# Kernel optimization log

Hardware: AMD Instinct MI355X
Metric: run time of the kernel (lower is better)

The kernel has to match this reference:

```python
import jax, jax.numpy as jnp
import numpy as np

B, S, NB = 8, 512, 23
INIT, E, R, T = 512, 256, 3, 2
NEG = -9e8

def _gru(x, h, wih, whh, bih, bhh):
    gi = x @ wih.T + bih
    gh = h @ whh.T + bhh
    ir, iz, inn = jnp.split(gi, 3, axis=-1)
    hr, hz, hn = jnp.split(gh, 3, axis=-1)
    r = jax.nn.sigmoid(ir + hr)
    z = jax.nn.sigmoid(iz + hz)
    n = jnp.tanh(inn + r * hn)
    return (1.0 - z) * n + z * h

def setup_inputs():
    key = jax.random.key(0)
    ks = jax.random.split(key, 30)
    def lin(k, o, i):
        return jax.random.normal(k, (o, i), jnp.float32) * 0.02
    def vec(k, n):
        return jax.random.normal(k, (n,), jnp.float32) * 0.02
    inp = {}
    inp["amino_list"] = jax.random.normal(ks[0], (B, S, INIT), jnp.float32)
    inp["amino_mask"] = (jax.random.uniform(ks[1], (B, S)) < 0.9).astype(jnp.float32)
    inp["emb_W"] = lin(ks[2], E, INIT); inp["emb_b"] = vec(ks[3], E)
    inp["nb_W"] = lin(ks[4], E, INIT); inp["nb_b"] = vec(ks[5], E)
    inp["align_W"] = jax.random.normal(ks[6], (R, 1, 2 * E), jnp.float32) * 0.02
    inp["align_b"] = jax.random.normal(ks[7], (R, 1), jnp.float32) * 0.02
    inp["attend_W"] = jax.random.normal(ks[8], (R, E, E), jnp.float32) * 0.02
    inp["attend_b"] = jax.random.normal(ks[9], (R, E), jnp.float32) * 0.02
    inp["gru_wih"] = jax.random.normal(ks[10], (R, 3 * E, E), jnp.float32) * 0.02
    inp["gru_whh"] = jax.random.normal(ks[11], (R, 3 * E, E), jnp.float32) * 0.02
    inp["gru_bih"] = jax.random.normal(ks[12], (R, 3 * E), jnp.float32) * 0.02
    inp["gru_bhh"] = jax.random.normal(ks[13], (R, 3 * E), jnp.float32) * 0.02
    inp["seq_align_W"] = lin(ks[14], 1, 2 * E); inp["seq_align_b"] = vec(ks[15], 1)
    inp["seq_attend_W"] = lin(ks[16], E, E); inp["seq_attend_b"] = vec(ks[17], E)
    inp["seq_gru_wih"] = lin(ks[18], 3 * E, E); inp["seq_gru_bih"] = vec(ks[19], 3 * E)
    inp["seq_gru_whh"] = lin(ks[20], 3 * E, E); inp["seq_gru_bhh"] = vec(ks[21], 3 * E)
    inp["amino_degree_list"] = jax.random.randint(ks[22], (B, S, NB), -1, S)
    return inp

def reference(amino_list, amino_mask, emb_W, emb_b, nb_W, nb_b, align_W, align_b,
              attend_W, attend_b, gru_wih, gru_whh, gru_bih, gru_bhh,
              seq_align_W, seq_align_b, seq_attend_W, seq_attend_b,
              seq_gru_wih, seq_gru_whh, seq_gru_bih, seq_gru_bhh, amino_degree_list):
    idx = amino_degree_list
    lrelu = jax.nn.leaky_relu
    # per-batch neighbor gather: (S,D),(S,NB) -> (S,NB,D); index -1 wraps (masked out below)
    gather = jax.vmap(lambda f, i: f[i])
    feat = lrelu(amino_list @ emb_W.T + emb_b)               # (B,S,E)
    nfeat = lrelu(gather(amino_list, idx) @ nb_W.T + nb_b)   # (B,S,NB,E)
    attend_mask = (idx != -1).astype(feat.dtype)             # (B,S,NB)
    smask = jnp.where(idx == -1, NEG, 0.0).astype(feat.dtype)

    def attn(d, center, nbr):
        # align Linear on concat([center, nbr]) split into two matvecs (same math, no concat)
        aW = align_W[d, 0]
        score = lrelu(jnp.einsum('bse,e->bs', center, aW[:E])[:, :, None]
                      + jnp.einsum('bsne,e->bsn', nbr, aW[E:]) + align_b[d, 0])
        w = jax.nn.softmax(score + smask, axis=-1) * attend_mask   # softmax over neighbor axis
        nt = nbr @ attend_W[d].T + attend_b[d]
        return jax.nn.elu(jnp.einsum('bsn,bsne->bse', w, nt))

    h = _gru(attn(0, feat, nfeat).reshape(-1, E), feat.reshape(-1, E),
             gru_wih[0], gru_whh[0], gru_bih[0], gru_bhh[0])
    act = jax.nn.relu(h.reshape(B, S, E))
    for d in range(1, R):
        ctx = attn(d, act, gather(act, idx))
        h = _gru(ctx.reshape(-1, E), h, gru_wih[d], gru_whh[d], gru_bih[d], gru_bhh[d])
        act = jax.nn.relu(h.reshape(B, S, E))

    seq_feature = jnp.sum(act * amino_mask[:, :, None], axis=1)  # (B,E)
    act_mol = jax.nn.relu(seq_feature)                           # fixed across T (as in torch)
    seq_smask = jnp.where(amino_mask == 0, NEG, 0.0)
    saW = seq_align_W[0]
    act_seq = act_mol
    for _ in range(T):
        score = lrelu((act_mol @ saW[:E])[:, None]
                      + jnp.einsum('bse,e->bs', act, saW[E:]) + seq_align_b[0])
        w = jax.nn.softmax(score + seq_smask, axis=-1) * amino_mask  # softmax over seq axis
        tf = act @ seq_attend_W.T + seq_attend_b
        seq_ctx = jax.nn.elu(jnp.einsum('bs,bse->be', w, tf))
        seq_feature = _gru(seq_ctx, seq_feature, seq_gru_wih, seq_gru_whh, seq_gru_bih, seq_gru_bhh)
        act_seq = jax.nn.relu(seq_feature)
    return (act_seq, act)
```

## Files before the change

### kernel.cpp

```cpp
#include <hip/hip_runtime.h>
#include <math.h>


#define BSZ   8
#define SEQ   512
#define NBR   23
#define EMB   256
#define INITD 512
#define BS    (BSZ*SEQ)
#define G3    (3*EMB)
#define NEGV  -9e8f

typedef __attribute__((ext_vector_type(8))) short short8;
typedef __attribute__((ext_vector_type(4))) float f32x4;

__device__ __forceinline__ float lrelu(float x){ return x > 0.f ? x : 0.01f*x; }
__device__ __forceinline__ float elu1 (float x){ return x > 0.f ? x : (expf(x)-1.f); }
__device__ __forceinline__ float sigm (float x){ return 1.f/(1.f+expf(-x)); }
__device__ __forceinline__ float bf2f(ushort u){
    union { unsigned int i; float f; } v; v.i = ((unsigned int)u) << 16; return v.f;
}
__device__ __forceinline__ ushort f2bf(float f){
    union { float f; unsigned int i; } v; v.f = f;
    unsigned int u = v.i;
    return (ushort)((u + 0x7FFFu + ((u >> 16) & 1u)) >> 16);
}

struct GemmLds { ushort A[2][64][64]; ushort W[2][64][64]; };

__global__ __launch_bounds__(256) void convert7_kernel(
    const float* s0, ushort* d0, int n0,
    const float* s1, ushort* d1, int n1,
    const float* s2, ushort* d2, int n2,
    const float* s3, ushort* d3, int n3,
    const float* s4, ushort* d4, int n4,
    const float* s5, ushort* d5, int n5,
    const float* s6, ushort* d6, int n6)
{
    const float* srcs[7] = {s0,s1,s2,s3,s4,s5,s6};
    ushort* dsts[7] = {d0,d1,d2,d3,d4,d5,d6};
    int ns[7] = {n0,n1,n2,n3,n4,n5,n6};
    int seg = blockIdx.y;
    const float* s = srcs[seg]; ushort* d = dsts[seg]; int n = ns[seg];
    size_t i = ((size_t)blockIdx.x * 256 + threadIdx.x) * 8;
    size_t stride = (size_t)gridDim.x * 256 * 8;
    for (; i < (size_t)n; i += stride) {
        float4 a = *reinterpret_cast<const float4*>(s + i);
        float4 b = *reinterpret_cast<const float4*>(s + i + 4);
        uint4 o;
        o.x = (unsigned)f2bf(a.x) | ((unsigned)f2bf(a.y) << 16);
        o.y = (unsigned)f2bf(a.z) | ((unsigned)f2bf(a.w) << 16);
        o.z = (unsigned)f2bf(b.x) | ((unsigned)f2bf(b.y) << 16);
        o.w = (unsigned)f2bf(b.z) | ((unsigned)f2bf(b.w) << 16);
        *reinterpret_cast<uint4*>(d + i) = o;
    }
}

template<int ACT, bool WF32, bool WBF>
__device__ __forceinline__ void gemm_dev(
    const ushort* __restrict__ A, const ushort* __restrict__ W,
    const float* __restrict__ bias,
    float* __restrict__ C, ushort* __restrict__ Cbf,
    int N, int K, int bx, int by, GemmLds& L)
{
    const int tid = threadIdx.x;
    const int m0 = bx * 64, n0 = by * 64;
    const int wv = tid >> 6, lane = tid & 63;
    const int fr = lane & 15, grp = lane >> 4;
    const int lrow = tid >> 3, lc8 = tid & 7;
    const int kc = K >> 3;
    const int sw = lc8 ^ (lrow & 7);

    f32x4 acc[4];
    #pragma unroll
    for (int c = 0; c < 4; ++c) acc[c] = (f32x4){0.f, 0.f, 0.f, 0.f};

    const float4* A4 = reinterpret_cast<const float4*>(A);
    const float4* W4 = reinterpret_cast<const float4*>(W);

    float4 a0 = A4[(size_t)(m0 + lrow)      * kc + lc8];
    float4 a1 = A4[(size_t)(m0 + lrow + 32) * kc + lc8];
    float4 w0 = W4[(size_t)(n0 + lrow)      * kc + lc8];
    float4 w1 = W4[(size_t)(n0 + lrow + 32) * kc + lc8];
    *reinterpret_cast<float4*>(&L.A[0][lrow     ][sw << 3]) = a0;
    *reinterpret_cast<float4*>(&L.A[0][lrow + 32][sw << 3]) = a1;
    *reinterpret_cast<float4*>(&L.W[0][lrow     ][sw << 3]) = w0;
    *reinterpret_cast<float4*>(&L.W[0][lrow + 32][sw << 3]) = w1;
    __syncthreads();

    const int ar = (wv << 4) + fr;
    int cur = 0;
    for (int k0 = 64; k0 < K; k0 += 64) {
        a0 = A4[(size_t)(m0 + lrow)      * kc + (k0 >> 3) + lc8];
        a1 = A4[(size_t)(m0 + lrow + 32) * kc + (k0 >> 3) + lc8];
        w0 = W4[(size_t)(n0 + lrow)      * kc + (k0 >> 3) + lc8];
        w1 = W4[(size_t)(n0 + lrow + 32) * kc + (k0 >> 3) + lc8];
        #pragma unroll
        for (int ks = 0; ks < 2; ++ks) {
            short8 af = *reinterpret_cast<const short8*>(
                &L.A[cur][ar][((((ks << 2) + grp) ^ (ar & 7)) << 3)]);
            #pragma unroll
            for (int c = 0; c < 4; ++c) {
                const int br = (c << 4) + fr;
                short8 bv = *reinterpret_cast<const short8*>(
                    &L.W[cur][br][((((ks << 2) + grp) ^ (br & 7)) << 3)]);
                acc[c] = __builtin_amdgcn_mfma_f32_16x16x32_bf16(af, bv, acc[c], 0, 0, 0);
            }
        }
        *reinterpret_cast<float4*>(&L.A[cur^1][lrow     ][sw << 3]) = a0;
        *reinterpret_cast<float4*>(&L.A[cur^1][lrow + 32][sw << 3]) = a1;
        *reinterpret_cast<float4*>(&L.W[cur^1][lrow     ][sw << 3]) = w0;
        *reinterpret_cast<float4*>(&L.W[cur^1][lrow + 32][sw << 3]) = w1;
        __syncthreads();
        cur ^= 1;
    }
    #pragma unroll
    for (int ks = 0; ks < 2; ++ks) {
        short8 af = *reinterpret_cast<const short8*>(
            &L.A[cur][ar][((((ks << 2) + grp) ^ (ar & 7)) << 3)]);
        #pragma unroll
        for (int c = 0; c < 4; ++c) {
            const int br = (c << 4) + fr;
            short8 bv = *reinterpret_cast<const short8*>(
                &L.W[cur][br][((((ks << 2) + grp) ^ (br & 7)) << 3)]);
            acc[c] = __builtin_amdgcn_mfma_f32_16x16x32_bf16(af, bv, acc[c], 0, 0, 0);
        }
    }

    const int mrow = m0 + (wv << 4) + (grp << 2);
    #pragma unroll
    for (int c = 0; c < 4; ++c) {
        const int n = n0 + (c << 4) + fr;
        const float bv = bias[n];
        #pragma unroll
        for (int j = 0; j < 4; ++j) {
            float t = acc[c][j] + bv;
            if (ACT == 1) t = lrelu(t);
            size_t off = (size_t)(mrow + j) * N + n;
            if (WF32) C[off] = t;
            if (WBF)  Cbf[off] = f2bf(t);
        }
    }
}

template<int ACT, bool WF32, bool WBF>
__global__ __launch_bounds__(256) void gemm_mfma(
    const ushort* __restrict__ A, const ushort* __restrict__ W,
    const float* __restrict__ bias,
    float* __restrict__ C, ushort* __restrict__ Cbf, int N, int K)
{
    __shared__ GemmLds L;
    gemm_dev<ACT,WF32,WBF>(A, W, bias, C, Cbf, N, K, blockIdx.x, blockIdx.y, L);
}

__global__ __launch_bounds__(256) void featnbase_kernel(
    const ushort* __restrict__ aminobf,
    const ushort* __restrict__ embWbf, const float* __restrict__ embB,
    float* __restrict__ feat, ushort* __restrict__ featbf,
    const ushort* __restrict__ nbWbf, const float* __restrict__ nbB,
    float* __restrict__ nbase, ushort* __restrict__ nbasebf)
{
    __shared__ GemmLds L;
    int blk = blockIdx.x;
    if (blk < 256)
        gemm_dev<1,true,true>(aminobf, embWbf, embB, feat, featbf, EMB, INITD, blk & 63, blk >> 6, L);
    else {
        blk -= 256;
        gemm_dev<1,true,true>(aminobf, nbWbf, nbB, nbase, nbasebf, EMB, INITD, blk & 63, blk >> 6, L);
    }
}

__global__ __launch_bounds__(256) void round_pre_kernel(
    const ushort* __restrict__ nbrbf, const ushort* __restrict__ attWd,
    const float* __restrict__ attBd, ushort* __restrict__ ntb,
    const ushort* __restrict__ hprevbf, const ushort* __restrict__ gwhhd,
    const float* __restrict__ gbhhd, float* __restrict__ gh,
    const float* __restrict__ center, const float* __restrict__ nbrbase,
    const float* __restrict__ alignWd,
    float* __restrict__ cdot, float* __restrict__ ndot)
{
    __shared__ GemmLds L;
    int blk = blockIdx.x;
    if (blk < 256) {
        gemm_dev<0,false,true>(nbrbf, attWd, attBd, nullptr, ntb, EMB, EMB, blk & 63, blk >> 6, L);
    } else if (blk < 1024) {
        int b = blk - 256;
        gemm_dev<0,true,false>(hprevbf, gwhhd, gbhhd, gh, nullptr, G3, EMB, b & 63, b >> 6, L);
    } else {
        const int b    = blk - 1024;
        const int lane = threadIdx.x & 63;
        const int wv   = threadIdx.x >> 6;
        const int e    = lane << 2;
        const int rb   = b * 16 + wv * 4;
        float4 w0 = *reinterpret_cast<const float4*>(&alignWd[e]);
        float4 w1 = *reinterpret_cast<const float4*>(&alignWd[EMB + e]);
        #pragma unroll
        for (int i = 0; i < 4; ++i) {
            const int r = rb + i;
            float4 xc = *reinterpret_cast<const float4*>(&center[(size_t)r*EMB + e]);
            float4 xn = *reinterpret_cast<const float4*>(&nbrbase[(size_t)r*EMB + e]);
            float ac = xc.x*w0.x + xc.y*w0.y + xc.z*w0.z + xc.w*w0.w;
            float an = xn.x*w1.x + xn.y*w1.y + xn.z*w1.z + xn.w*w1.w;
            #pragma unroll
            for (int off = 32; off; off >>= 1) {
                ac += __shfl_xor(ac, off, 64);
                an += __shfl_xor(an, off, 64);
            }
            if (lane == 0) { cdot[r] = ac; ndot[r] = an; }
        }
    }
}

__global__ __launch_bounds__(256) void attn_kernel(
    const float* __restrict__ cdot, const float* __restrict__ ndot,
    const int* __restrict__ idx, const ushort* __restrict__ nt,
    const float* __restrict__ alignB, ushort* __restrict__ ctxbf)
{
    const int r   = blockIdx.x;
    const int b   = r >> 9;
    const int tid = threadIdx.x;
    __shared__ float w_s[NBR];
    __shared__ float vm_s[NBR];
    __shared__ int   row_s[NBR];
    __shared__ float red[2];
    if (tid < NBR) {
        int j = idx[(size_t)r*NBR + tid];
        int valid = (j >= 0);
        int jj = valid ? j : j + SEQ;
        int row = b*SEQ + jj;
        row_s[tid] = row;
        vm_s[tid]  = (float)valid;
        float sc = lrelu(cdot[r] + ndot[row] + alignB[0]);
        w_s[tid] = sc + (valid ? 0.f : NEGV);
    }
    __syncthreads();
    if (tid == 0) {
        float m = w_s[0];
        for (int n = 1; n < NBR; ++n) m = fmaxf(m, w_s[n]);
        red[0] = m;
    }
    __syncthreads();
    if (tid < NBR) w_s[tid] = expf(w_s[tid] - red[0]);
    __syncthreads();
    if (tid == 0) {
        float s = 0.f;
        for (int n = 0; n < NBR; ++n) s += w_s[n];
        red[1] = 1.f / s;
    }
    __syncthreads();
    if (tid < NBR) w_s[tid] *= red[1] * vm_s[tid];
    __syncthreads();
    float acc = 0.f;
    #pragma unroll 1
    for (int n = 0; n < NBR; ++n)
        acc += w_s[n] * bf2f(nt[(size_t)row_s[n]*EMB + tid]);
    ctxbf[(size_t)r*EMB + tid] = f2bf(elu1(acc));
}

__global__ __launch_bounds__(256) void gru_kernel(
    const float* __restrict__ gi, const float* __restrict__ gh,
    const float* __restrict__ hprev,
    float* __restrict__ hout, ushort* __restrict__ hbf,
    float* __restrict__ actout, ushort* __restrict__ actbf)
{
    const size_t r = blockIdx.x * 4 + (threadIdx.x >> 6);
    const int    e = (threadIdx.x & 63) << 2;
    const size_t gb = r*G3 + e, hb = r*EMB + e;
    float4 ir4 = *reinterpret_cast<const float4*>(&gi[gb]);
    float4 iz4 = *reinterpret_cast<const float4*>(&gi[gb + EMB]);
    float4 in4 = *reinterpret_cast<const float4*>(&gi[gb + 2*EMB]);
    float4 hr4 = *reinterpret_cast<const float4*>(&gh[gb]);
    float4 hz4 = *reinterpret_cast<const float4*>(&gh[gb + EMB]);
    float4 hn4 = *reinterpret_cast<const float4*>(&gh[gb + 2*EMB]);
    float4 hp4 = *reinterpret_cast<const float4*>(&hprev[hb]);
    float hv[4], av[4];
    const float ir_[4] = {ir4.x,ir4.y,ir4.z,ir4.w}, iz_[4] = {iz4.x,iz4.y,iz4.z,iz4.w},
                in_[4] = {in4.x,in4.y,in4.z,in4.w}, hr_[4] = {hr4.x,hr4.y,hr4.z,hr4.w},
                hz_[4] = {hz4.x,hz4.y,hz4.z,hz4.w}, hn_[4] = {hn4.x,hn4.y,hn4.z,hn4.w},
                hp_[4] = {hp4.x,hp4.y,hp4.z,hp4.w};
    #pragma unroll
    for (int i = 0; i < 4; ++i) {
        float rg = sigm(ir_[i] + hr_[i]);
        float z  = sigm(iz_[i] + hz_[i]);
        float n  = tanhf(in_[i] + rg*hn_[i]);
        hv[i] = (1.f - z)*n + z*hp_[i];
        av[i] = fmaxf(hv[i], 0.f);
    }
    *reinterpret_cast<float4*>(&hout[hb])   = make_float4(hv[0],hv[1],hv[2],hv[3]);
    *reinterpret_cast<float4*>(&actout[hb]) = make_float4(av[0],av[1],av[2],av[3]);
    uint2 hp, ap;
    hp.x = (unsigned)f2bf(hv[0]) | ((unsigned)f2bf(hv[1]) << 16);
    hp.y = (unsigned)f2bf(hv[2]) | ((unsigned)f2bf(hv[3]) << 16);
    ap.x = (unsigned)f2bf(av[0]) | ((unsigned)f2bf(av[1]) << 16);
    ap.y = (unsigned)f2bf(av[2]) | ((unsigned)f2bf(av[3]) << 16);
    *reinterpret_cast<uint2*>(&hbf[hb])  = hp;
    *reinterpret_cast<uint2*>(&actbf[hb]) = ap;
}

__global__ __launch_bounds__(256) void seqpre_kernel(
    const ushort* __restrict__ actbf, const ushort* __restrict__ satWbf,
    const float* __restrict__ satB, float* __restrict__ tf,
    const float* __restrict__ act, const float* __restrict__ mask,
    const float* __restrict__ saW,
    float* __restrict__ seqfeat, float* __restrict__ cmol,
    float* __restrict__ ad)
{
    __shared__ GemmLds L;
    int blk = blockIdx.x;
    if (blk < 256) {
        gemm_dev<0,true,false>(actbf, satWbf, satB, tf, nullptr, EMB, EMB, blk & 63, blk >> 6, L);
    } else if (blk < 264) {
        const int b = blk - 256;
        const int e = threadIdx.x;
        float acc = 0.f;
        for (int s = 0; s < SEQ; ++s)
            acc += act[((size_t)b*SEQ + s)*EMB + e] * mask[b*SEQ + s];
        seqfeat[b*EMB + e] = acc;
        float* red = reinterpret_cast<float*>(&L);
        red[e] = fmaxf(acc, 0.f) * saW[e];
        __syncthreads();
        for (int off = 128; off; off >>= 1) {
            if (e < off) red[e] += red[e + off];
            __syncthreads();
        }
        if (e == 0) cmol[b] = red[0];
    } else {
        const int b2   = blk - 264;
        const int lane = threadIdx.x & 63;
        const int wv   = threadIdx.x >> 6;
        const int e    = lane << 2;
        const int rb   = b2 * 16 + wv * 4;
        float4 w1 = *reinterpret_cast<const float4*>(&saW[EMB + e]);
        #pragma unroll
        for (int i = 0; i < 4; ++i) {
            const int r = rb + i;
            float4 xa = *reinterpret_cast<const float4*>(&act[(size_t)r*EMB + e]);
            float an = xa.x*w1.x + xa.y*w1.y + xa.z*w1.z + xa.w*w1.w;
            #pragma unroll
            for (int off = 32; off; off >>= 1) an += __shfl_xor(an, off, 64);
            if (lane == 0) ad[r] = an;
        }
    }
}

__global__ __launch_bounds__(512) void seqsoftmax_kernel(
    const float* __restrict__ ad, const float* __restrict__ mask,
    const float* __restrict__ saB, const float* __restrict__ cmol,
    float* __restrict__ wvec)
{
    const int b = blockIdx.x;
    const int s = threadIdx.x;
    __shared__ float red[SEQ];
    float mk = mask[b*SEQ + s];
    float sc = lrelu(cmol[b] + ad[b*SEQ + s] + saB[0]) + (mk == 0.f ? NEGV : 0.f);
    red[s] = sc; __syncthreads();
    for (int off = 256; off; off >>= 1) {
        if (s < off) red[s] = fmaxf(red[s], red[s + off]);
        __syncthreads();
    }
    float m = red[0]; __syncthreads();
    float ev = expf(sc - m);
    red[s] = ev; __syncthreads();
    for (int off = 256; off; off >>= 1) {
        if (s < off) red[s] += red[s + off];
        __syncthreads();
    }
    wvec[b*SEQ + s] = ev / red[0] * mk;
}

__global__ __launch_bounds__(256) void seqpv_kernel(
    const float* __restrict__ wvec, const float* __restrict__ tf,
    float* __restrict__ partial)
{
    const int st = blockIdx.x, b = blockIdx.y;
    const int e  = threadIdx.x;
    float acc = 0.f;
    const int s0 = st * 32;
    #pragma unroll 4
    for (int s = s0; s < s0 + 32; ++s)
        acc += wvec[b*SEQ + s] * tf[((size_t)b*SEQ + s)*EMB + e];
    partial[((size_t)b*16 + st)*EMB + e] = acc;
}

__global__ __launch_bounds__(256) void seqfinish_kernel(
    const float* __restrict__ partial, float* __restrict__ seqctx)
{
    const int b = blockIdx.x, e = threadIdx.x;
    float acc = 0.f;
    #pragma unroll
    for (int st = 0; st < 16; ++st)
        acc += partial[((size_t)b*16 + st)*EMB + e];
    seqctx[(size_t)b*EMB + e] = elu1(acc);
}

__global__ __launch_bounds__(256) void matvec8_kernel(
    const float* __restrict__ X, const float* __restrict__ Wm,
    const float* __restrict__ bias, float* __restrict__ Y)
{
    const int g    = blockIdx.x * 4 + (threadIdx.x >> 6);
    const int b    = blockIdx.y;
    const int lane = threadIdx.x & 63;
    float4 w = *reinterpret_cast<const float4*>(&Wm[(size_t)g*EMB + (lane << 2)]);
    float4 x = *reinterpret_cast<const float4*>(&X[(size_t)b*EMB + (lane << 2)]);
    float d = w.x*x.x + w.y*x.y + w.z*x.z + w.w*x.w;
    #pragma unroll
    for (int off = 32; off; off >>= 1) d += __shfl_xor(d, off, 64);
    if (lane == 0) Y[(size_t)b*G3 + g] = d + bias[g];
}

__global__ __launch_bounds__(256) void seqgru_el_kernel(
    const float* __restrict__ sgi, const float* __restrict__ sgh,
    const float* __restrict__ sfin,
    float* __restrict__ sfout, float* __restrict__ actseq)
{
    const int b = blockIdx.x;
    const int e = threadIdx.x;
    float rg = sigm(sgi[b*G3 + e]       + sgh[b*G3 + e]);
    float z  = sigm(sgi[b*G3 + EMB + e] + sgh[b*G3 + EMB + e]);
    float n  = tanhf(sgi[b*G3 + 2*EMB + e] + rg * sgh[b*G3 + 2*EMB + e]);
    float hp = sfin[b*EMB + e];
    float hv = (1.f - z)*n + z*hp;
    sfout[b*EMB + e]  = hv;
    actseq[b*EMB + e] = fmaxf(hv, 0.f);
}

extern "C" void kernel_launch(void* const* d_in, const int* in_sizes, int n_in,
                              void* d_out, int out_size, void* d_ws, size_t ws_size,
                              hipStream_t stream) {
    (void)in_sizes; (void)n_in; (void)out_size; (void)ws_size;
    const float* amino  = (const float*)d_in[0];
    const float* mask   = (const float*)d_in[1];
    const float* embW   = (const float*)d_in[2];
    const float* embB   = (const float*)d_in[3];
    const float* nbW    = (const float*)d_in[4];
    const float* nbB    = (const float*)d_in[5];
    const float* alignW = (const float*)d_in[6];
    const float* alignB = (const float*)d_in[7];
    const float* attW   = (const float*)d_in[8];
    const float* attB   = (const float*)d_in[9];
    const float* gwih   = (const float*)d_in[10];
    const float* gwhh   = (const float*)d_in[11];
    const float* gbih   = (const float*)d_in[12];
    const float* gbhh   = (const float*)d_in[13];
    const float* saW    = (const float*)d_in[14];
    const float* saB    = (const float*)d_in[15];
    const float* satW   = (const float*)d_in[16];
    const float* satB   = (const float*)d_in[17];
    const float* sgwih  = (const float*)d_in[18];
    const float* sgbih  = (const float*)d_in[19];
    const float* sgwhh  = (const float*)d_in[20];
    const float* sgbhh  = (const float*)d_in[21];
    const int*   idx    = (const int*)d_in[22];

    char* cur = (char*)d_ws;
    auto alloc = [&](size_t bytes) -> char* {
        char* p = cur; cur += (bytes + 255) & ~(size_t)255; return p;
    };
    float* feat    = (float*)alloc((size_t)BS*EMB*4);
    float* nbase   = (float*)alloc((size_t)BS*EMB*4);
    float* h       = (float*)alloc((size_t)BS*EMB*4);
    float* gi      = (float*)alloc((size_t)BS*G3*4);
    float* gh      = (float*)alloc((size_t)BS*G3*4);
    float* cdot    = (float*)alloc(BS*4);
    float* ndot    = (float*)alloc(BS*4);
    float* seqfeat = (float*)alloc(BSZ*EMB*4);
    float* cmol    = (float*)alloc(64*4);
    float* seqctx  = (float*)alloc(BSZ*EMB*4);
    float* sgi     = (float*)alloc(BSZ*G3*4);
    float* sgh     = (float*)alloc(BSZ*G3*4);
    float* partial = (float*)alloc((size_t)BSZ*16*EMB*4);
    ushort* featbf  = (ushort*)alloc((size_t)BS*EMB*2);
    ushort* nbasebf = (ushort*)alloc((size_t)BS*EMB*2);
    ushort* actbf   = (ushort*)alloc((size_t)BS*EMB*2);
    ushort* hbf     = (ushort*)alloc((size_t)BS*EMB*2);
    ushort* ctxbf   = (ushort*)alloc((size_t)BS*EMB*2);
    ushort* ntb     = (ushort*)alloc((size_t)BS*EMB*2);
    ushort* embWbf  = (ushort*)alloc((size_t)EMB*INITD*2);
    ushort* nbWbf   = (ushort*)alloc((size_t)EMB*INITD*2);
    ushort* attWbf  = (ushort*)alloc((size_t)3*EMB*EMB*2);
    ushort* gwihbf  = (ushort*)alloc((size_t)3*G3*EMB*2);
    ushort* gwhhbf  = (ushort*)alloc((size_t)3*G3*EMB*2);
    ushort* satWbf  = (ushort*)alloc((size_t)EMB*EMB*2);
    ushort* aminobf = (ushort*)gi;
    float*  tf      = gi;
    float*  ad      = cdot;
    float*  wvec    = ndot;

    float* out    = (float*)d_out;
    float* actseq = out;
    float* act    = out + BSZ*EMB;

    convert7_kernel<<<dim3(1024, 7), 256, 0, stream>>>(
        amino, aminobf, BS*INITD,
        embW,  embWbf,  EMB*INITD,
        nbW,   nbWbf,   EMB*INITD,
        attW,  attWbf,  3*EMB*EMB,
        gwih,  gwihbf,  3*G3*EMB,
        gwhh,  gwhhbf,  3*G3*EMB,
        satW,  satWbf,  EMB*EMB);

    featnbase_kernel<<<512, 256, 0, stream>>>(
        aminobf, embWbf, embB, feat, featbf, nbWbf, nbB, nbase, nbasebf);

    for (int d = 0; d < 3; ++d) {
        const float*  center   = (d == 0) ? feat    : act;
        const float*  nbrbase  = (d == 0) ? nbase   : act;
        const ushort* nbrbf    = (d == 0) ? nbasebf : actbf;
        const float*  hprev    = (d == 0) ? feat    : h;
        const ushort* hprevbf  = (d == 0) ? featbf  : hbf;
        round_pre_kernel<<<1280, 256, 0, stream>>>(
            nbrbf, attWbf + (size_t)d*EMB*EMB, attB + d*EMB, ntb,
            hprevbf, gwhhbf + (size_t)d*G3*EMB, gbhh + d*G3, gh,
            center, nbrbase, alignW + d*2*EMB, cdot, ndot);
        attn_kernel<<<BS, 256, 0, stream>>>(cdot, ndot, idx, ntb, alignB + d, ctxbf);
        gemm_mfma<0,true,false><<<dim3(64, 12), 256, 0, stream>>>(
            ctxbf, gwihbf + (size_t)d*G3*EMB, gbih + d*G3, gi, nullptr, G3, EMB);
        gru_kernel<<<BS/4, 256, 0, stream>>>(gi, gh, hprev, h, hbf, act, actbf);
    }

    seqpre_kernel<<<520, 256, 0, stream>>>(
        actbf, satWbf, satB, tf, act, mask, saW, seqfeat, cmol, ad);
    seqsoftmax_kernel<<<BSZ, 512, 0, stream>>>(ad, mask, saB, cmol, wvec);
    seqpv_kernel<<<dim3(16, BSZ), 256, 0, stream>>>(wvec, tf, partial);
    seqfinish_kernel<<<BSZ, 256, 0, stream>>>(partial, seqctx);
    matvec8_kernel<<<dim3(G3/4, BSZ), 256, 0, stream>>>(seqctx, sgwih, sgbih, sgi);
    for (int t = 0; t < 2; ++t) {
        matvec8_kernel<<<dim3(G3/4, BSZ), 256, 0, stream>>>(seqfeat, sgwhh, sgbhh, sgh);
        seqgru_el_kernel<<<BSZ, 256, 0, stream>>>(sgi, sgh, seqfeat, seqfeat, actseq);
    }
}
```

Measured before the change: 184.2 us.

## Store GRU gates in bf16, warp-per-row attention, fuse sequence tail kernels

The gi/gh gate buffers are now written and read in bf16 instead of fp32, halving the traffic of the largest intermediates. The neighbour-attention kernel now processes four rows per block, one wavefront per row, using shuffles instead of shared-memory serial reductions, and reads vectorised ushort4 values. The sequence-level tail merges softmax, PV and finish into fewer kernels, and replaces the matvec/GRU chain with two fused seqstep kernels that use bf16 weights converted up front. Together these cut launch count and memory traffic, at the cost of extra bf16 rounding on the gate pre-activations and the sequence GRU weights.

```diff
diff --git a/kernel.cpp b/kernel.cpp
--- a/kernel.cpp
+++ b/kernel.cpp
@@ -28,18 +28,20 @@
 
 struct GemmLds { ushort A[2][64][64]; ushort W[2][64][64]; };
 
-__global__ __launch_bounds__(256) void convert7_kernel(
+__global__ __launch_bounds__(256) void convert9_kernel(
     const float* s0, ushort* d0, int n0,
     const float* s1, ushort* d1, int n1,
     const float* s2, ushort* d2, int n2,
     const float* s3, ushort* d3, int n3,
     const float* s4, ushort* d4, int n4,
     const float* s5, ushort* d5, int n5,
-    const float* s6, ushort* d6, int n6)
-{
-    const float* srcs[7] = {s0,s1,s2,s3,s4,s5,s6};
-    ushort* dsts[7] = {d0,d1,d2,d3,d4,d5,d6};
-    int ns[7] = {n0,n1,n2,n3,n4,n5,n6};
+    const float* s6, ushort* d6, int n6,
+    const float* s7, ushort* d7, int n7,
+    const float* s8, ushort* d8, int n8)
+{
+    const float* srcs[9] = {s0,s1,s2,s3,s4,s5,s6,s7,s8};
+    ushort* dsts[9] = {d0,d1,d2,d3,d4,d5,d6,d7,d8};
+    int ns[9] = {n0,n1,n2,n3,n4,n5,n6,n7,n8};
     int seg = blockIdx.y;
     const float* s = srcs[seg]; ushort* d = dsts[seg]; int n = ns[seg];
     size_t i = ((size_t)blockIdx.x * 256 + threadIdx.x) * 8;
@@ -174,7 +176,7 @@
     const ushort* __restrict__ nbrbf, const ushort* __restrict__ attWd,
     const float* __restrict__ attBd, ushort* __restrict__ ntb,
     const ushort* __restrict__ hprevbf, const ushort* __restrict__ gwhhd,
-    const float* __restrict__ gbhhd, float* __restrict__ gh,
+    const float* __restrict__ gbhhd, ushort* __restrict__ ghbf,
     const float* __restrict__ center, const float* __restrict__ nbrbase,
     const float* __restrict__ alignWd,
     float* __restrict__ cdot, float* __restrict__ ndot)
@@ -185,7 +187,7 @@
         gemm_dev<0,false,true>(nbrbf, attWd, attBd, nullptr, ntb, EMB, EMB, blk & 63, blk >> 6, L);
     } else if (blk < 1024) {
         int b = blk - 256;
-        gemm_dev<0,true,false>(hprevbf, gwhhd, gbhhd, gh, nullptr, G3, EMB, b & 63, b >> 6, L);
+        gemm_dev<0,false,true>(hprevbf, gwhhd, gbhhd, nullptr, ghbf, G3, EMB, b & 63, b >> 6, L);
     } else {
         const int b    = blk - 1024;
         const int lane = threadIdx.x & 63;
@@ -216,49 +218,44 @@
     const int* __restrict__ idx, const ushort* __restrict__ nt,
     const float* __restrict__ alignB, ushort* __restrict__ ctxbf)
 {
-    const int r   = blockIdx.x;
-    const int b   = r >> 9;
-    const int tid = threadIdx.x;
-    __shared__ float w_s[NBR];
-    __shared__ float vm_s[NBR];
-    __shared__ int   row_s[NBR];
-    __shared__ float red[2];
-    if (tid < NBR) {
-        int j = idx[(size_t)r*NBR + tid];
+    const int lane = threadIdx.x & 63;
+    const int r = blockIdx.x * 4 + (threadIdx.x >> 6);
+    const int b = r >> 9;
+    float sc = -3e38f, vm = 0.f; int row = 0;
+    if (lane < NBR) {
+        int j = idx[(size_t)r*NBR + lane];
         int valid = (j >= 0);
         int jj = valid ? j : j + SEQ;
-        int row = b*SEQ + jj;
-        row_s[tid] = row;
-        vm_s[tid]  = (float)valid;
-        float sc = lrelu(cdot[r] + ndot[row] + alignB[0]);
-        w_s[tid] = sc + (valid ? 0.f : NEGV);
-    }
-    __syncthreads();
-    if (tid == 0) {
-        float m = w_s[0];
-        for (int n = 1; n < NBR; ++n) m = fmaxf(m, w_s[n]);
-        red[0] = m;
-    }
-    __syncthreads();
-    if (tid < NBR) w_s[tid] = expf(w_s[tid] - red[0]);
-    __syncthreads();
-    if (tid == 0) {
-        float s = 0.f;
-        for (int n = 0; n < NBR; ++n) s += w_s[n];
-        red[1] = 1.f / s;
-    }
-    __syncthreads();
-    if (tid < NBR) w_s[tid] *= red[1] * vm_s[tid];
-    __syncthreads();
-    float acc = 0.f;
+        row = b*SEQ + jj;
+        vm = (float)valid;
+        sc = lrelu(cdot[r] + ndot[row] + alignB[0]) + (valid ? 0.f : NEGV);
+    }
+    float m = sc;
+    #pragma unroll
+    for (int off = 32; off; off >>= 1) m = fmaxf(m, __shfl_xor(m, off, 64));
+    float ev = (lane < NBR) ? expf(sc - m) : 0.f;
+    float s = ev;
+    #pragma unroll
+    for (int off = 32; off; off >>= 1) s += __shfl_xor(s, off, 64);
+    float wgt = ev * vm / s;
+    float acc0 = 0.f, acc1 = 0.f, acc2 = 0.f, acc3 = 0.f;
+    const int e = lane << 2;
     #pragma unroll 1
-    for (int n = 0; n < NBR; ++n)
-        acc += w_s[n] * bf2f(nt[(size_t)row_s[n]*EMB + tid]);
-    ctxbf[(size_t)r*EMB + tid] = f2bf(elu1(acc));
+    for (int n = 0; n < NBR; ++n) {
+        float wn = __shfl(wgt, n, 64);
+        int   rn = __shfl(row, n, 64);
+        ushort4 v = *reinterpret_cast<const ushort4*>(&nt[(size_t)rn*EMB + e]);
+        acc0 += wn * bf2f(v.x); acc1 += wn * bf2f(v.y);
+        acc2 += wn * bf2f(v.z); acc3 += wn * bf2f(v.w);
+    }
+    uint2 o;
+    o.x = (unsigned)f2bf(elu1(acc0)) | ((unsigned)f2bf(elu1(acc1)) << 16);
+    o.y = (unsigned)f2bf(elu1(acc2)) | ((unsigned)f2bf(elu1(acc3)) << 16);
+    *reinterpret_cast<uint2*>(&ctxbf[(size_t)r*EMB + e]) = o;
 }
 
 __global__ __launch_bounds__(256) void gru_kernel(
-    const float* __restrict__ gi, const float* __restrict__ gh,
+    const ushort* __restrict__ gibf, const ushort* __restrict__ ghbf,
     const float* __restrict__ hprev,
     float* __restrict__ hout, ushort* __restrict__ hbf,
     float* __restrict__ actout, ushort* __restrict__ actbf)
@@ -266,18 +263,21 @@
     const size_t r = blockIdx.x * 4 + (threadIdx.x >> 6);
     const int    e = (threadIdx.x & 63) << 2;
     const size_t gb = r*G3 + e, hb = r*EMB + e;
-    float4 ir4 = *reinterpret_cast<const float4*>(&gi[gb]);
-    float4 iz4 = *reinterpret_cast<const float4*>(&gi[gb + EMB]);
-    float4 in4 = *reinterpret_cast<const float4*>(&gi[gb + 2*EMB]);
-    float4 hr4 = *reinterpret_cast<const float4*>(&gh[gb]);
-    float4 hz4 = *reinterpret_cast<const float4*>(&gh[gb + EMB]);
-    float4 hn4 = *reinterpret_cast<const float4*>(&gh[gb + 2*EMB]);
+    ushort4 ir4 = *reinterpret_cast<const ushort4*>(&gibf[gb]);
+    ushort4 iz4 = *reinterpret_cast<const ushort4*>(&gibf[gb + EMB]);
+    ushort4 in4 = *reinterpret_cast<const ushort4*>(&gibf[gb + 2*EMB]);
+    ushort4 hr4 = *reinterpret_cast<const ushort4*>(&ghbf[gb]);
+    ushort4 hz4 = *reinterpret_cast<const ushort4*>(&ghbf[gb + EMB]);
+    ushort4 hn4 = *reinterpret_cast<const ushort4*>(&ghbf[gb + 2*EMB]);
     float4 hp4 = *reinterpret_cast<const float4*>(&hprev[hb]);
+    const float ir_[4] = {bf2f(ir4.x),bf2f(ir4.y),bf2f(ir4.z),bf2f(ir4.w)};
+    const float iz_[4] = {bf2f(iz4.x),bf2f(iz4.y),bf2f(iz4.z),bf2f(iz4.w)};
+    const float in_[4] = {bf2f(in4.x),bf2f(in4.y),bf2f(in4.z),bf2f(in4.w)};
+    const float hr_[4] = {bf2f(hr4.x),bf2f(hr4.y),bf2f(hr4.z),bf2f(hr4.w)};
+    const float hz_[4] = {bf2f(hz4.x),bf2f(hz4.y),bf2f(hz4.z),bf2f(hz4.w)};
+    const float hn_[4] = {bf2f(hn4.x),bf2f(hn4.y),bf2f(hn4.z),bf2f(hn4.w)};
+    const float hp_[4] = {hp4.x,hp4.y,hp4.z,hp4.w};
     float hv[4], av[4];
-    const float ir_[4] = {ir4.x,ir4.y,ir4.z,ir4.w}, iz_[4] = {iz4.x,iz4.y,iz4.z,iz4.w},
-                in_[4] = {in4.x,in4.y,in4.z,in4.w}, hr_[4] = {hr4.x,hr4.y,hr4.z,hr4.w},
-                hz_[4] = {hz4.x,hz4.y,hz4.z,hz4.w}, hn_[4] = {hn4.x,hn4.y,hn4.z,hn4.w},
-                hp_[4] = {hp4.x,hp4.y,hp4.z,hp4.w};
     #pragma unroll
     for (int i = 0; i < 4; ++i) {
         float rg = sigm(ir_[i] + hr_[i]);
@@ -293,7 +293,7 @@
     hp.y = (unsigned)f2bf(hv[2]) | ((unsigned)f2bf(hv[3]) << 16);
     ap.x = (unsigned)f2bf(av[0]) | ((unsigned)f2bf(av[1]) << 16);
     ap.y = (unsigned)f2bf(av[2]) | ((unsigned)f2bf(av[3]) << 16);
-    *reinterpret_cast<uint2*>(&hbf[hb])  = hp;
+    *reinterpret_cast<uint2*>(&hbf[hb])   = hp;
     *reinterpret_cast<uint2*>(&actbf[hb]) = ap;
 }
 
@@ -343,85 +343,106 @@
     }
 }
 
-__global__ __launch_bounds__(512) void seqsoftmax_kernel(
+__global__ __launch_bounds__(256) void seqpv2_kernel(
     const float* __restrict__ ad, const float* __restrict__ mask,
     const float* __restrict__ saB, const float* __restrict__ cmol,
-    float* __restrict__ wvec)
-{
-    const int b = blockIdx.x;
-    const int s = threadIdx.x;
-    __shared__ float red[SEQ];
-    float mk = mask[b*SEQ + s];
-    float sc = lrelu(cmol[b] + ad[b*SEQ + s] + saB[0]) + (mk == 0.f ? NEGV : 0.f);
-    red[s] = sc; __syncthreads();
-    for (int off = 256; off; off >>= 1) {
-        if (s < off) red[s] = fmaxf(red[s], red[s + off]);
+    const float* __restrict__ tf, float* __restrict__ partial)
+{
+    const int st = blockIdx.x, b = blockIdx.y;
+    const int tid = threadIdx.x;
+    __shared__ float w_s[SEQ];
+    __shared__ float red[256];
+    float mk0 = mask[b*SEQ + tid], mk1 = mask[b*SEQ + 256 + tid];
+    float cb = cmol[b], bb = saB[0];
+    float s0 = lrelu(cb + ad[b*SEQ + tid] + bb)       + (mk0 == 0.f ? NEGV : 0.f);
+    float s1 = lrelu(cb + ad[b*SEQ + 256 + tid] + bb) + (mk1 == 0.f ? NEGV : 0.f);
+    red[tid] = fmaxf(s0, s1); __syncthreads();
+    for (int off = 128; off; off >>= 1) {
+        if (tid < off) red[tid] = fmaxf(red[tid], red[tid + off]);
         __syncthreads();
     }
     float m = red[0]; __syncthreads();
-    float ev = expf(sc - m);
-    red[s] = ev; __syncthreads();
-    for (int off = 256; off; off >>= 1) {
-        if (s < off) red[s] += red[s + off];
+    float e0 = expf(s0 - m), e1 = expf(s1 - m);
+    red[tid] = e0 + e1; __syncthreads();
+    for (int off = 128; off; off >>= 1) {
+        if (tid < off) red[tid] += red[tid + off];
         __syncthreads();
     }
-    wvec[b*SEQ + s] = ev / red[0] * mk;
-}
-
-__global__ __launch_bounds__(256) void seqpv_kernel(
-    const float* __restrict__ wvec, const float* __restrict__ tf,
-    float* __restrict__ partial)
-{
-    const int st = blockIdx.x, b = blockIdx.y;
-    const int e  = threadIdx.x;
+    float inv = 1.f / red[0];
+    w_s[tid]       = e0 * inv * mk0;
+    w_s[tid + 256] = e1 * inv * mk1;
+    __syncthreads();
     float acc = 0.f;
-    const int s0 = st * 32;
+    const int s0i = st * 32;
     #pragma unroll 4
-    for (int s = s0; s < s0 + 32; ++s)
-        acc += wvec[b*SEQ + s] * tf[((size_t)b*SEQ + s)*EMB + e];
-    partial[((size_t)b*16 + st)*EMB + e] = acc;
-}
-
-__global__ __launch_bounds__(256) void seqfinish_kernel(
-    const float* __restrict__ partial, float* __restrict__ seqctx)
-{
-    const int b = blockIdx.x, e = threadIdx.x;
-    float acc = 0.f;
-    #pragma unroll
-    for (int st = 0; st < 16; ++st)
-        acc += partial[((size_t)b*16 + st)*EMB + e];
-    seqctx[(size_t)b*EMB + e] = elu1(acc);
-}
-
-__global__ __launch_bounds__(256) void matvec8_kernel(
-    const float* __restrict__ X, const float* __restrict__ Wm,
-    const float* __restrict__ bias, float* __restrict__ Y)
-{
-    const int g    = blockIdx.x * 4 + (threadIdx.x >> 6);
-    const int b    = blockIdx.y;
-    const int lane = threadIdx.x & 63;
-    float4 w = *reinterpret_cast<const float4*>(&Wm[(size_t)g*EMB + (lane << 2)]);
-    float4 x = *reinterpret_cast<const float4*>(&X[(size_t)b*EMB + (lane << 2)]);
-    float d = w.x*x.x + w.y*x.y + w.z*x.z + w.w*x.w;
-    #pragma unroll
-    for (int off = 32; off; off >>= 1) d += __shfl_xor(d, off, 64);
-    if (lane == 0) Y[(size_t)b*G3 + g] = d + bias[g];
-}
-
-__global__ __launch_bounds__(256) void seqgru_el_kernel(
-    const float* __restrict__ sgi, const float* __restrict__ sgh,
-    const float* __restrict__ sfin,
-    float* __restrict__ sfout, float* __restrict__ actseq)
-{
-    const int b = blockIdx.x;
-    const int e = threadIdx.x;
-    float rg = sigm(sgi[b*G3 + e]       + sgh[b*G3 + e]);
-    float z  = sigm(sgi[b*G3 + EMB + e] + sgh[b*G3 + EMB + e]);
-    float n  = tanhf(sgi[b*G3 + 2*EMB + e] + rg * sgh[b*G3 + 2*EMB + e]);
-    float hp = sfin[b*EMB + e];
-    float hv = (1.f - z)*n + z*hp;
-    sfout[b*EMB + e]  = hv;
-    actseq[b*EMB + e] = fmaxf(hv, 0.f);
+    for (int s = s0i; s < s0i + 32; ++s)
+        acc += w_s[s] * tf[((size_t)b*SEQ + s)*EMB + tid];
+    partial[((size_t)b*16 + st)*EMB + tid] = acc;
+}
+
+template<int T0>
+__global__ __launch_bounds__(512) void seqstep_kernel(
+    const float* __restrict__ partial, const float* __restrict__ sfin,
+    const ushort* __restrict__ sgwihbf, const float* __restrict__ sgbih,
+    const ushort* __restrict__ sgwhhbf, const float* __restrict__ sgbhh,
+    float* __restrict__ sgi, float* __restrict__ sfout,
+    float* __restrict__ actseq)
+{
+    const int b = blockIdx.x >> 2, q = blockIdx.x & 3;
+    const int tid = threadIdx.x, lane = tid & 63, wv = tid >> 6;
+    __shared__ float xs[EMB];
+    __shared__ float hs[EMB];
+    __shared__ float gis[192], ghs[192];
+    if (tid < EMB) {
+        hs[tid] = sfin[b*EMB + tid];
+        if (T0) {
+            float a = 0.f;
+            #pragma unroll
+            for (int st = 0; st < 16; ++st)
+                a += partial[((size_t)b*16 + st)*EMB + tid];
+            xs[tid] = elu1(a);
+        }
+    }
+    if (!T0) {
+        for (int l = tid; l < 192; l += 512) {
+            int g = (l >> 6)*EMB + (q << 6) + (l & 63);
+            gis[l] = sgi[b*G3 + g];
+        }
+    }
+    __syncthreads();
+    const int nrows = T0 ? 384 : 192;
+    const int rpw = nrows >> 3;
+    for (int i = 0; i < rpw; ++i) {
+        const int l = wv * rpw + i;
+        const int iswih = T0 && (l < 192);
+        const int ll = (T0 && l >= 192) ? l - 192 : l;
+        const int g = (ll >> 6)*EMB + (q << 6) + (ll & 63);
+        const ushort* Wm = iswih ? sgwihbf : sgwhhbf;
+        ushort4 w4 = *reinterpret_cast<const ushort4*>(&Wm[(size_t)g*EMB + (lane << 2)]);
+        float4 x4 = *reinterpret_cast<const float4*>(iswih ? &xs[lane << 2] : &hs[lane << 2]);
+        float d = bf2f(w4.x)*x4.x + bf2f(w4.y)*x4.y + bf2f(w4.z)*x4.z + bf2f(w4.w)*x4.w;
+        #pragma unroll
+        for (int off = 32; off; off >>= 1) d += __shfl_xor(d, off, 64);
+        if (lane == 0) {
+            if (iswih) {
+                d += sgbih[g];
+                gis[ll] = d;
+                sgi[b*G3 + g] = d;
+            } else {
+                ghs[ll] = d + sgbhh[g];
+            }
+        }
+    }
+    __syncthreads();
+    if (tid < 64) {
+        const int e = (q << 6) + tid;
+        float rg = sigm(gis[tid]       + ghs[tid]);
+        float z  = sigm(gis[64 + tid]  + ghs[64 + tid]);
+        float n  = tanhf(gis[128 + tid] + rg*ghs[128 + tid]);
+        float hv = (1.f - z)*n + z*hs[e];
+        sfout[b*EMB + e]  = hv;
+        actseq[b*EMB + e] = fmaxf(hv, 0.f);
+    }
 }
 
 extern "C" void kernel_launch(void* const* d_in, const int* in_sizes, int n_in,
@@ -459,45 +480,47 @@
     float* feat    = (float*)alloc((size_t)BS*EMB*4);
     float* nbase   = (float*)alloc((size_t)BS*EMB*4);
     float* h       = (float*)alloc((size_t)BS*EMB*4);
-    float* gi      = (float*)alloc((size_t)BS*G3*4);
-    float* gh      = (float*)alloc((size_t)BS*G3*4);
+    float* tf      = (float*)alloc((size_t)BS*EMB*4);
     float* cdot    = (float*)alloc(BS*4);
     float* ndot    = (float*)alloc(BS*4);
+    float* ad      = (float*)alloc(BS*4);
     float* seqfeat = (float*)alloc(BSZ*EMB*4);
+    float* sf2     = (float*)alloc(BSZ*EMB*4);
     float* cmol    = (float*)alloc(64*4);
-    float* seqctx  = (float*)alloc(BSZ*EMB*4);
     float* sgi     = (float*)alloc(BSZ*G3*4);
-    float* sgh     = (float*)alloc(BSZ*G3*4);
     float* partial = (float*)alloc((size_t)BSZ*16*EMB*4);
+    ushort* aminobf = (ushort*)alloc((size_t)BS*INITD*2);
     ushort* featbf  = (ushort*)alloc((size_t)BS*EMB*2);
     ushort* nbasebf = (ushort*)alloc((size_t)BS*EMB*2);
     ushort* actbf   = (ushort*)alloc((size_t)BS*EMB*2);
     ushort* hbf     = (ushort*)alloc((size_t)BS*EMB*2);
     ushort* ctxbf   = (ushort*)alloc((size_t)BS*EMB*2);
     ushort* ntb     = (ushort*)alloc((size_t)BS*EMB*2);
+    ushort* gibf    = (ushort*)alloc((size_t)BS*G3*2);
+    ushort* ghbf    = (ushort*)alloc((size_t)BS*G3*2);
     ushort* embWbf  = (ushort*)alloc((size_t)EMB*INITD*2);
     ushort* nbWbf   = (ushort*)alloc((size_t)EMB*INITD*2);
     ushort* attWbf  = (ushort*)alloc((size_t)3*EMB*EMB*2);
     ushort* gwihbf  = (ushort*)alloc((size_t)3*G3*EMB*2);
     ushort* gwhhbf  = (ushort*)alloc((size_t)3*G3*EMB*2);
     ushort* satWbf  = (ushort*)alloc((size_t)EMB*EMB*2);
-    ushort* aminobf = (ushort*)gi;
-    float*  tf      = gi;
-    float*  ad      = cdot;
-    float*  wvec    = ndot;
+    ushort* sgwihbf = (ushort*)alloc((size_t)G3*EMB*2);
+    ushort* sgwhhbf = (ushort*)alloc((size_t)G3*EMB*2);
 
     float* out    = (float*)d_out;
     float* actseq = out;
     float* act    = out + BSZ*EMB;
 
-    convert7_kernel<<<dim3(1024, 7), 256, 0, stream>>>(
+    convert9_kernel<<<dim3(1024, 9), 256, 0, stream>>>(
         amino, aminobf, BS*INITD,
         embW,  embWbf,  EMB*INITD,
         nbW,   nbWbf,   EMB*INITD,
         attW,  attWbf,  3*EMB*EMB,
         gwih,  gwihbf,  3*G3*EMB,
         gwhh,  gwhhbf,  3*G3*EMB,
-        satW,  satWbf,  EMB*EMB);
+        satW,  satWbf,  EMB*EMB,
+        sgwih, sgwihbf, G3*EMB,
+        sgwhh, sgwhhbf, G3*EMB);
 
     featnbase_kernel<<<512, 256, 0, stream>>>(
         aminobf, embWbf, embB, feat, featbf, nbWbf, nbB, nbase, nbasebf);
@@ -510,22 +533,19 @@
         const ushort* hprevbf  = (d == 0) ? featbf  : hbf;
         round_pre_kernel<<<1280, 256, 0, stream>>>(
             nbrbf, attWbf + (size_t)d*EMB*EMB, attB + d*EMB, ntb,
-            hprevbf, gwhhbf + (size_t)d*G3*EMB, gbhh + d*G3, gh,
+            hprevbf, gwhhbf + (size_t)d*G3*EMB, gbhh + d*G3, ghbf,
             center, nbrbase, alignW + d*2*EMB, cdot, ndot);
-        attn_kernel<<<BS, 256, 0, stream>>>(cdot, ndot, idx, ntb, alignB + d, ctxbf);
-        gemm_mfma<0,true,false><<<dim3(64, 12), 256, 0, stream>>>(
-            ctxbf, gwihbf + (size_t)d*G3*EMB, gbih + d*G3, gi, nullptr, G3, EMB);
-        gru_kernel<<<BS/4, 256, 0, stream>>>(gi, gh, hprev, h, hbf, act, actbf);
+        attn_kernel<<<BS/4, 256, 0, stream>>>(cdot, ndot, idx, ntb, alignB + d, ctxbf);
+        gemm_mfma<0,false,true><<<dim3(64, 12), 256, 0, stream>>>(
+            ctxbf, gwihbf + (size_t)d*G3*EMB, gbih + d*G3, nullptr, gibf, G3, EMB);
+        gru_kernel<<<BS/4, 256, 0, stream>>>(gibf, ghbf, hprev, h, hbf, act, actbf);
     }
 
     seqpre_kernel<<<520, 256, 0, stream>>>(
         actbf, satWbf, satB, tf, act, mask, saW, seqfeat, cmol, ad);
-    seqsoftmax_kernel<<<BSZ, 512, 0, stream>>>(ad, mask, saB, cmol, wvec);
-    seqpv_kernel<<<dim3(16, BSZ), 256, 0, stream>>>(wvec, tf, partial);
-    seqfinish_kernel<<<BSZ, 256, 0, stream>>>(partial, seqctx);
-    matvec8_kernel<<<dim3(G3/4, BSZ), 256, 0, stream>>>(seqctx, sgwih, sgbih, sgi);
-    for (int t = 0; t < 2; ++t) {
-        matvec8_kernel<<<dim3(G3/4, BSZ), 256, 0, stream>>>(seqfeat, sgwhh, sgbhh, sgh);
-        seqgru_el_kernel<<<BSZ, 256, 0, stream>>>(sgi, sgh, seqfeat, seqfeat, actseq);
-    }
-}
+    seqpv2_kernel<<<dim3(16, BSZ), 256, 0, stream>>>(ad, mask, saB, cmol, tf, partial);
+    seqstep_kernel<1><<<32, 512, 0, stream>>>(
+        partial, seqfeat, sgwihbf, sgbih, sgwhhbf, sgbhh, sgi, sf2, actseq);
+    seqstep_kernel<0><<<32, 512, 0, stream>>>(
+        partial, sf2, sgwihbf, sgbih, sgwhhbf, sgbhh, sgi, seqfeat, actseq);
+}
```

After: 187.8 us. Within noise of the previous version (+2.0%).
